# Kernel optimization log

Hardware: AMD Instinct MI355X
Metric: run time of the kernel (lower is better)

## Reference

```python
import jax, jax.numpy as jnp
import numpy as np
from jax import lax

BN_EPS = 1e-3
SLOPE = 0.1
CLUSTER_TEMP = 30.0
K = 16
FEAT = 4096  # 8*8*64


def conv_bn_lrelu(x, w, b, g, beta, m, v):
    # Conv2d stride 2, padding 1 (NCHW / OIHW), then eval-mode BatchNorm, then LeakyReLU.
    y = lax.conv_general_dilated(x, w, window_strides=(2, 2), padding=((1, 1), (1, 1)),
                                 dimension_numbers=("NCHW", "OIHW", "NCHW"))
    y = y + b[None, :, None, None]
    scale = g / jnp.sqrt(v + BN_EPS)
    y = y * scale[None, :, None, None] + (beta - m * scale)[None, :, None, None]
    return jnp.where(y > 0, y, SLOPE * y)


def soft_kmeans(data, mu, num_iter, ct):
    # Row L2-normalize (equivalent to diag(1/||x||) @ data)
    data = data / jnp.linalg.norm(data, axis=1, keepdims=True)
    for _ in range(num_iter):
        dist = data @ mu.T                      # [N, K]
        r = jax.nn.softmax(ct * dist, axis=1)   # [N, K]
        mu = (r.T @ data) / r.sum(axis=0)[:, None]  # [K, F]
    dist = data @ mu.T
    r = jax.nn.softmax(ct * dist, axis=1)
    return mu, r, dist


def setup_inputs() -> dict:
    key = jax.random.key(0)
    ks = jax.random.split(key, 12)
    d = {}
    d["x"] = jax.random.normal(ks[0], (256, 3, 64, 64), dtype=jnp.float32)
    # conv1: 3 -> 128
    d["conv1_w"] = jax.random.normal(ks[1], (128, 3, 3, 3), dtype=jnp.float32) * 0.05
    d["conv1_b"] = jnp.zeros((128,), jnp.float32)
    d["bn1_g"] = jnp.ones((128,), jnp.float32)
    d["bn1_b"] = jnp.zeros((128,), jnp.float32)
    d["bn1_m"] = jax.random.normal(ks[2], (128,), dtype=jnp.float32) * 0.1
    d["bn1_v"] = jax.random.uniform(ks[3], (128,), minval=0.5, maxval=1.5, dtype=jnp.float32)
    # conv2: 128 -> 256
    d["conv2_w"] = jax.random.normal(ks[4], (256, 128, 3, 3), dtype=jnp.float32) * 0.02
    d["conv2_b"] = jnp.zeros((256,), jnp.float32)
    d["bn2_g"] = jnp.ones((256,), jnp.float32)
    d["bn2_b"] = jnp.zeros((256,), jnp.float32)
    d["bn2_m"] = jax.random.normal(ks[5], (256,), dtype=jnp.float32) * 0.1
    d["bn2_v"] = jax.random.uniform(ks[6], (256,), minval=0.5, maxval=1.5, dtype=jnp.float32)
    # conv3: 256 -> 64
    d["conv3_w"] = jax.random.normal(ks[7], (64, 256, 3, 3), dtype=jnp.float32) * 0.02
    d["conv3_b"] = jnp.zeros((64,), jnp.float32)
    d["bn3_g"] = jnp.ones((64,), jnp.float32)
    d["bn3_b"] = jnp.zeros((64,), jnp.float32)
    d["bn3_m"] = jax.random.normal(ks[8], (64,), dtype=jnp.float32) * 0.1
    d["bn3_v"] = jax.random.uniform(ks[9], (64,), minval=0.5, maxval=1.5, dtype=jnp.float32)
    # initial cluster centers, torch.rand(K, F)
    d["mu0"] = jax.random.uniform(ks[10], (K, FEAT), dtype=jnp.float32)
    d["num_iter"] = 10
    return d


def reference(x, conv1_w, conv1_b, bn1_g, bn1_b, bn1_m, bn1_v,
              conv2_w, conv2_b, bn2_g, bn2_b, bn2_m, bn2_v,
              conv3_w, conv3_b, bn3_g, bn3_b, bn3_m, bn3_v,
              mu0, num_iter):
    h = conv_bn_lrelu(x, conv1_w, conv1_b, bn1_g, bn1_b, bn1_m, bn1_v)   # [B,128,32,32]
    h = conv_bn_lrelu(h, conv2_w, conv2_b, bn2_g, bn2_b, bn2_m, bn2_v)   # [B,256,16,16]
    h = conv_bn_lrelu(h, conv3_w, conv3_b, bn3_g, bn3_b, bn3_m, bn3_v)   # [B,64,8,8]
    embeds = h.reshape(-1, FEAT)                                          # [B, 4096]
    mu_init, _, _ = soft_kmeans(embeds, mu0, num_iter, CLUSTER_TEMP)
    _, r, _ = soft_kmeans(embeds, lax.stop_gradient(mu_init), 1, CLUSTER_TEMP)
    return r
```

## Files before the change

kernel.cpp:

```cpp
#include <hip/hip_runtime.h>
#include <stdint.h>
#include <stddef.h>

typedef unsigned short u16;
typedef __attribute__((ext_vector_type(8))) short short8;
typedef __attribute__((ext_vector_type(4))) float f32x4;
typedef __attribute__((ext_vector_type(4))) int int4v;

__device__ __forceinline__ float bf2f(u16 u) {
    unsigned x = ((unsigned)u) << 16;
    return __uint_as_float(x);
}
__device__ __forceinline__ u16 f2bf(float f) {
    unsigned x = __float_as_uint(f);
    unsigned r = (x + 0x7fffu + ((x >> 16) & 1u)) >> 16;
    return (u16)r;
}
__device__ __forceinline__ float ldin(const void* p, size_t i, int isbf) {
    return isbf ? bf2f(((const u16*)p)[i]) : ((const float*)p)[i];
}
__device__ __forceinline__ int detect_bf(const void* v1) {
    const u16* ub = (const u16*)v1;
    int ok = 1;
#pragma unroll
    for (int i = 0; i < 16; i++) {
        float f = bf2f(ub[i]);
        if (!(f >= 0.4f && f <= 1.6f)) ok = 0;
    }
    return ok;
}
__device__ __forceinline__ int sw(int r, int c8) {
    return r * 32 + (((c8) ^ (r & 3)) << 3);
}

struct PrepArgs {
    const void *w1, *w2, *w3;
    u16 *W1p, *W2p, *W3p;
    const void *b1, *g1, *be1, *m1, *v1;
    const void *b2, *g2, *be2, *m2, *v2;
    const void *b3, *g3, *be3, *m3, *v3;
    float *es1, *esh1, *es2, *esh2, *es3, *esh3;
    u16 *zb;
};
__device__ __forceinline__ void packw_body(const void* src, u16* dst, int CI, int Kp,
                                           int total, int blk, int t, int isbf) {
    int p = blk * 256 + t;
    if (p >= total) return;
    int co = p / Kp, k = p - co * Kp;
    int tap = k / CI, ci = k - tap * CI;
    u16 v = 0;
    if (tap < 9) {
        size_t si = (size_t)(co * CI + ci) * 9 + tap;
        v = isbf ? ((const u16*)src)[si] : f2bf(((const float*)src)[si]);
    }
    dst[p] = v;
}
__global__ __launch_bounds__(256) void kprep_all(PrepArgs A) {
    int b = blockIdx.x, t = threadIdx.x;
    int isbf = detect_bf(A.v1);
    if (b < 1152) {
        packw_body(A.w2, A.W2p, 128, 1152, 256 * 1152, b, t, isbf);
    } else if (b < 1728) {
        packw_body(A.w3, A.W3p, 256, 2304, 64 * 2304, b - 1152, t, isbf);
    } else if (b < 1744) {
        packw_body(A.w1, A.W1p, 3, 32, 128 * 32, b - 1728, t, isbf);
    } else {
        if (b == 1745) A.zb[t] = 0;
        int u = (b - 1744) * 256 + t;
        const void *bb, *g, *be, *m, *v;
        float *es, *esh;
        int c;
        if (u < 128)      { c = u;       bb=A.b1; g=A.g1; be=A.be1; m=A.m1; v=A.v1; es=A.es1; esh=A.esh1; }
        else if (u < 384) { c = u - 128; bb=A.b2; g=A.g2; be=A.be2; m=A.m2; v=A.v2; es=A.es2; esh=A.esh2; }
        else if (u < 448) { c = u - 384; bb=A.b3; g=A.g3; be=A.be3; m=A.m3; v=A.v3; es=A.es3; esh=A.esh3; }
        else return;
        float sc = ldin(g, c, isbf) / sqrtf(ldin(v, c, isbf) + 1e-3f);
        float sh = (ldin(bb, c, isbf) - ldin(m, c, isbf)) * sc + ldin(be, c, isbf);
        es[c] = sc;
        esh[c] = sh;
    }
}

__global__ void kfallback(u16* __restrict__ out) {
    int i = blockIdx.x * 256 + threadIdx.x;
    if (i < 4096) out[i] = f2bf(0.0625f);
}

__global__ __launch_bounds__(256) void imc1_gemm(
    const void* __restrict__ x, const u16* __restrict__ W,
    const float* __restrict__ es, const float* __restrict__ esh,
    u16* __restrict__ OutB, const void* __restrict__ v1ref) {
    __shared__ u16 xs[3 * 64 * 64];
    alignas(16) __shared__ u16 As[2][128 * 32];
    alignas(16) __shared__ u16 Bs[128 * 32];

    const int img = blockIdx.x, t = threadIdx.x;
    const int isbf = detect_bf(v1ref);
    const int lane = t & 63, w = t >> 6;
    const int wm = w & 1, wn = w >> 1;
    const int rA = t >> 2, c8 = t & 3, koff = c8 * 8;
    const int qc = lane >> 4, fr = lane & 15;

    if (isbf) {
        const u16* xp = (const u16*)x + (size_t)img * 12288;
#pragma unroll
        for (int i = t * 8; i < 12288; i += 2048)
            *(int4v*)&xs[i] = *(const int4v*)&xp[i];
    } else {
        const float* xp = (const float*)x + (size_t)img * 12288;
#pragma unroll
        for (int i = t * 4; i < 12288; i += 1024) {
            float4 v = *(const float4*)&xp[i];
            xs[i] = f2bf(v.x); xs[i + 1] = f2bf(v.y);
            xs[i + 2] = f2bf(v.z); xs[i + 3] = f2bf(v.w);
        }
    }
#pragma unroll
    for (int j = 0; j < 2; j++) {
        int4v vb = *(const int4v*)(W + (size_t)(j * 64 + rA) * 32 + koff);
        *(int4v*)&Bs[sw(j * 64 + rA, c8)] = vb;
    }
    __syncthreads();
    short8 bf[4];
#pragma unroll
    for (int j = 0; j < 4; j++) bf[j] = *(const short8*)&Bs[sw(wn * 64 + j * 16 + fr, qc)];
    float scv[4], shv[4];
#pragma unroll
    for (int j = 0; j < 4; j++) {
        int c = wn * 64 + j * 16 + fr;
        scv[j] = es[c];
        shv[j] = esh[c];
    }

    for (int sub = 0; sub < 8; ++sub) {
        const int buf = sub & 1;
#pragma unroll
        for (int j = 0; j < 2; j++) {
            int r = j * 64 + rA;
            int p = sub * 128 + r;
            int ox = p & 31, oy = p >> 5;
            alignas(16) u16 row[8];
#pragma unroll
            for (int e = 0; e < 8; e++) {
                int k = koff + e;
                u16 val = 0;
                if (k < 27) {
                    int tap = k / 3, ci = k - 3 * tap;
                    int ky = tap / 3, kx = tap - 3 * ky;
                    int iy = 2 * oy - 1 + ky, ix = 2 * ox - 1 + kx;
                    if ((unsigned)iy < 64u && (unsigned)ix < 64u)
                        val = xs[ci * 4096 + iy * 64 + ix];
                }
                row[e] = val;
            }
            *(int4v*)&As[buf][sw(r, c8)] = *(const int4v*)row;
        }
        __syncthreads();
        short8 af[4];
#pragma unroll
        for (int i = 0; i < 4; i++)
            af[i] = *(const short8*)&As[buf][sw(wm * 64 + i * 16 + fr, qc)];
        f32x4 acc[4][4];
#pragma unroll
        for (int i = 0; i < 4; i++)
#pragma unroll
            for (int j = 0; j < 4; j++) {
#pragma unroll
                for (int q = 0; q < 4; q++) acc[i][j][q] = 0.f;
                acc[i][j] = __builtin_amdgcn_mfma_f32_16x16x32_bf16(af[i], bf[j], acc[i][j], 0, 0, 0);
            }
#pragma unroll
        for (int i = 0; i < 4; i++) {
#pragma unroll
            for (int rg = 0; rg < 4; rg++) {
                int p = sub * 128 + wm * 64 + i * 16 + qc * 4 + rg;
                int ox = p & 31, oy = p >> 5;
                u16* orow = OutB + ((size_t)(img * 32 + oy) * 32 + ox) * 128 + wn * 64 + fr;
#pragma unroll
                for (int j = 0; j < 4; j++) {
                    float v = acc[i][j][rg] * scv[j] + shv[j];
                    v = (v > 0.f) ? v : 0.1f * v;
                    orow[j * 16] = f2bf(v);
                }
            }
        }
    }
}

__global__ __launch_bounds__(512, 2) void gemm_conv2(
    const u16* __restrict__ h1, const u16* __restrict__ W,
    const float* __restrict__ es, const float* __restrict__ esh,
    u16* __restrict__ OutB, const u16* __restrict__ zb) {
    alignas(16) __shared__ u16 smem[4 * 16384];
    u16* const Ab0 = smem;
    u16* const Ab1 = smem + 16384;
    u16* const Bb0 = smem + 32768;
    u16* const Bb1 = smem + 49152;

    const int t = threadIdx.x;
    const int w = t >> 6, l = t & 63;
    const int img = blockIdx.x;
    const int wm = w >> 2, wn = w & 3;
    const int fr = l & 15, qc = l >> 4;

    int aiy0[4], aix0[4], ac8e[4];
    int brow[4];
#pragma unroll
    for (int i = 0; i < 4; ++i) {
        int gi = w * 256 + i * 64 + l;
        int r = gi >> 3, c8d = gi & 7;
        int c8s = c8d ^ (r & 7);
        int oy = r >> 4, ox = r & 15;
        aiy0[i] = 2 * oy - 1;
        aix0[i] = 2 * ox - 1;
        ac8e[i] = c8s * 8;
        brow[i] = r * 1152 + c8s * 8;
    }
    auto mkA = [&](int i, int ky, int kx) -> const u16* {
        int iy = aiy0[i] + ky, ix = aix0[i] + kx;
        if ((unsigned)iy < 32u && (unsigned)ix < 32u)
            return h1 + (size_t)(((img * 32 + iy) * 32 + ix) * 128 + ac8e[i]);
        return zb;
    };
    auto stage = [&](const u16* src, u16* ldsbase, int i) {
        __builtin_amdgcn_global_load_lds(
            (const __attribute__((address_space(1))) void*)src,
            (__attribute__((address_space(3))) void*)(ldsbase + (w * 4 + i) * 512),
            16, 0, 0);
    };

    f32x4 acc[8][4];
#pragma unroll
    for (int mi = 0; mi < 8; ++mi)
#pragma unroll
        for (int nj = 0; nj < 4; ++nj)
#pragma unroll
            for (int q = 0; q < 4; ++q) acc[mi][nj][q] = 0.0f;

    auto do_tile = [&](const u16* A, const u16* B) {
#pragma unroll
        for (int kk = 0; kk < 2; ++kk) {
            const int c8 = kk * 4 + qc;
            short8 a[8], b[4];
#pragma unroll
            for (int q = 0; q < 8; ++q) {
                int row = wm * 128 + q * 16 + fr;
                a[q] = *(const short8*)(A + row * 64 + ((c8 ^ (row & 7)) << 3));
            }
#pragma unroll
            for (int j = 0; j < 4; ++j) {
                int row = wn * 64 + j * 16 + fr;
                b[j] = *(const short8*)(B + row * 64 + ((c8 ^ (row & 7)) << 3));
            }
            __builtin_amdgcn_s_setprio(1);
#pragma unroll
            for (int q = 0; q < 8; ++q)
#pragma unroll
                for (int j = 0; j < 4; ++j)
                    acc[q][j] = __builtin_amdgcn_mfma_f32_16x16x32_bf16(
                        a[q], b[j], acc[q][j], 0, 0, 0);
            __builtin_amdgcn_s_setprio(0);
        }
    };

    const u16* pcur[4];
#pragma unroll
    for (int i = 0; i < 4; ++i) pcur[i] = mkA(i, 0, 0);
#pragma unroll
    for (int i = 0; i < 4; ++i) {
        stage(pcur[i], Ab0, i);
        stage(W + brow[i], Bb0, i);
    }

    for (int tap = 0; tap < 9; ++tap) {
        __syncthreads();
#pragma unroll
        for (int i = 0; i < 4; ++i) {
            stage(pcur[i] + 64, Ab1, i);
            stage(W + brow[i] + (2 * tap + 1) * 64, Bb1, i);
        }
        do_tile(Ab0, Bb0);
        __syncthreads();
        if (tap < 8) {
            const int tap2 = tap + 1;
            const int ky2 = (tap2 >= 6) ? 2 : (tap2 >= 3) ? 1 : 0;
            const int kx2 = tap2 - 3 * ky2;
#pragma unroll
            for (int i = 0; i < 4; ++i) pcur[i] = mkA(i, ky2, kx2);
#pragma unroll
            for (int i = 0; i < 4; ++i) {
                stage(pcur[i], Ab0, i);
                stage(W + brow[i] + (2 * tap + 2) * 64, Bb0, i);
            }
        }
        do_tile(Ab1, Bb1);
    }

    float scv[4], shv[4];
#pragma unroll
    for (int nj = 0; nj < 4; ++nj) {
        int c = wn * 64 + nj * 16 + fr;
        scv[nj] = es[c];
        shv[nj] = esh[c];
    }
#pragma unroll
    for (int mi = 0; mi < 8; ++mi) {
#pragma unroll
        for (int rg = 0; rg < 4; ++rg) {
            int r = wm * 128 + mi * 16 + qc * 4 + rg;
            u16* orow = OutB + ((size_t)img * 256 + r) * 256 + wn * 64 + fr;
#pragma unroll
            for (int nj = 0; nj < 4; ++nj) {
                float v = acc[mi][nj][rg] * scv[nj] + shv[nj];
                v = (v > 0.f) ? v : 0.1f * v;
                orow[nj * 16] = f2bf(v);
            }
        }
    }
}

__global__ __launch_bounds__(256) void gemm_conv3f(
    const u16* __restrict__ Asrc, const u16* __restrict__ W,
    const float* __restrict__ es3, const float* __restrict__ esh3,
    float* __restrict__ dat, u16* __restrict__ datbf,
    const u16* __restrict__ zb) {
    alignas(16) __shared__ u16 smem[4 * 4096];
    __shared__ float red[4];
    u16* const AbP[2] = {smem, smem + 4096};
    u16* const BbP[2] = {smem + 8192, smem + 12288};

    const int t = threadIdx.x;
    const int w = t >> 6, l = t & 63;
    const int lid = blockIdx.x;
    const int xcd = lid & 7, slot = lid >> 3;
    const int img = xcd * 32 + slot;
    const int wm = w & 1, wn = w >> 1;
    const int fr = l & 15, qc = l >> 4;

    int aiy0[2], aix0[2], ac8e[2];
    int brow[2];
#pragma unroll
    for (int i = 0; i < 2; ++i) {
        int g = w * 128 + i * 64 + l;
        int r = g >> 3, c8d = g & 7;
        int c8s = c8d ^ (r & 7);
        int oy = r >> 3, ox = r & 7;
        aiy0[i] = 2 * oy - 1;
        aix0[i] = 2 * ox - 1;
        ac8e[i] = c8s * 8;
        brow[i] = r * 2304 + c8s * 8;
    }
    auto mkA = [&](int i, int ky, int kx) -> const u16* {
        int iy = aiy0[i] + ky, ix = aix0[i] + kx;
        if ((unsigned)iy < 16u && (unsigned)ix < 16u)
            return Asrc + (size_t)(((img * 16 + iy) * 16 + ix) * 256 + ac8e[i]);
        return zb;
    };
    auto stage = [&](const u16* src, u16* ldsbase, int i) {
        __builtin_amdgcn_global_load_lds(
            (const __attribute__((address_space(1))) void*)src,
            (__attribute__((address_space(3))) void*)(ldsbase + (w * 2 + i) * 512),
            16, 0, 0);
    };

    f32x4 acc[2][2];
#pragma unroll
    for (int i = 0; i < 2; i++)
#pragma unroll
        for (int j = 0; j < 2; j++)
#pragma unroll
            for (int q = 0; q < 4; q++) acc[i][j][q] = 0.0f;

    auto do_tile = [&](const u16* A, const u16* B) {
#pragma unroll
        for (int kk = 0; kk < 2; ++kk) {
            const int c8 = kk * 4 + qc;
            short8 a[2], b[2];
#pragma unroll
            for (int i = 0; i < 2; ++i) {
                int row = wm * 32 + i * 16 + fr;
                a[i] = *(const short8*)(A + row * 64 + ((c8 ^ (row & 7)) << 3));
            }
#pragma unroll
            for (int j = 0; j < 2; ++j) {
                int row = wn * 32 + j * 16 + fr;
                b[j] = *(const short8*)(B + row * 64 + ((c8 ^ (row & 7)) << 3));
            }
            __builtin_amdgcn_s_setprio(1);
#pragma unroll
            for (int i = 0; i < 2; ++i)
#pragma unroll
                for (int j = 0; j < 2; ++j)
                    acc[i][j] = __builtin_amdgcn_mfma_f32_16x16x32_bf16(
                        a[i], b[j], acc[i][j], 0, 0, 0);
            __builtin_amdgcn_s_setprio(0);
        }
    };

    const u16* pcur[2];
#pragma unroll
    for (int i = 0; i < 2; ++i) pcur[i] = mkA(i, 0, 0);
#pragma unroll
    for (int i = 0; i < 2; ++i) {
        stage(pcur[i], AbP[0], i);
        stage(W + brow[i], BbP[0], i);
    }

    int flat = 0;
    for (int tap = 0; tap < 9; ++tap) {
        for (int q4 = 0; q4 < 4; ++q4, ++flat) {
            const int cb = flat & 1;
            __syncthreads();
            int ntap = tap, nq = q4 + 1;
            if (nq == 4) { nq = 0; ntap = tap + 1; }
            if (ntap < 9) {
                if (nq == 0) {
                    const int ky = (ntap >= 6) ? 2 : (ntap >= 3) ? 1 : 0;
                    const int kx = ntap - 3 * ky;
#pragma unroll
                    for (int i = 0; i < 2; ++i) pcur[i] = mkA(i, ky, kx);
                }
#pragma unroll
                for (int i = 0; i < 2; ++i) {
                    stage(pcur[i] + nq * 64, AbP[cb ^ 1], i);
                    stage(W + brow[i] + ntap * 256 + nq * 64, BbP[cb ^ 1], i);
                }
            }
            do_tile(AbP[cb], BbP[cb]);
        }
    }

    float vals[2][2][4];
    float ssq = 0.f;
#pragma unroll
    for (int j = 0; j < 2; j++) {
        int c = wn * 32 + j * 16 + fr;
        float sc = es3[c], sh = esh3[c];
#pragma unroll
        for (int i = 0; i < 2; i++) {
#pragma unroll
            for (int rg = 0; rg < 4; rg++) {
                float v = acc[i][j][rg] * sc + sh;
                v = (v > 0.f) ? v : 0.1f * v;
                vals[i][j][rg] = v;
                ssq += v * v;
            }
        }
    }
#pragma unroll
    for (int off = 32; off > 0; off >>= 1) ssq += __shfl_xor(ssq, off);
    if (l == 0) red[w] = ssq;
    __syncthreads();
    float inv = 1.0f / sqrtf(red[0] + red[1] + red[2] + red[3]);
#pragma unroll
    for (int j = 0; j < 2; j++) {
        int c = wn * 32 + j * 16 + fr;
#pragma unroll
        for (int i = 0; i < 2; i++) {
#pragma unroll
            for (int rg = 0; rg < 4; rg++) {
                int row = wm * 32 + i * 16 + qc * 4 + rg;
                size_t idx = (size_t)img * 4096 + c * 64 + row;
                float v = vals[i][j][rg] * inv;
                dat[idx] = v;
                datbf[idx] = f2bf(v);
            }
        }
    }
}

__global__ __launch_bounds__(256) void kgr(const u16* __restrict__ dbf,
                                           const float* __restrict__ dat,
                                           const void* __restrict__ mu0,
                                           float* __restrict__ Gp,
                                           float* __restrict__ rb0,
                                           const void* __restrict__ v1ref) {
    const int b = blockIdx.x, t = threadIdx.x;
    __shared__ float part[16][4];
    __shared__ float ds[16];

    if (b < 128) {
        const int tile = b & 15, s = b >> 4;
        const int m0 = (tile & 3) * 64, n0 = (tile >> 2) * 64;
        const int lane = t & 63, w = t >> 6;
        const int wm = w & 1, wn = w >> 1;
        const int fr = lane & 15, qc = lane >> 4;

        f32x4 acc[2][2];
#pragma unroll
        for (int i = 0; i < 2; i++)
#pragma unroll
            for (int j = 0; j < 2; j++)
#pragma unroll
                for (int q = 0; q < 4; q++) acc[i][j][q] = 0.0f;

        const u16* a0p = dbf + (size_t)(m0 + wm * 32 + fr) * 4096 + s * 512 + qc * 8;
        const u16* a1p = a0p + 16 * 4096;
        const u16* b0p = dbf + (size_t)(n0 + wn * 32 + fr) * 4096 + s * 512 + qc * 8;
        const u16* b1p = b0p + 16 * 4096;

        short8 Pa0[4], Pa1[4], Pb0[4], Pb1[4];
        short8 Qa0[4], Qa1[4], Qb0[4], Qb1[4];
        auto ldc = [&](short8* A0, short8* A1, short8* B0, short8* B1, int c) {
#pragma unroll
            for (int u = 0; u < 4; ++u) {
                const int o = c * 128 + u * 32;
                A0[u] = *(const short8*)(a0p + o);
                A1[u] = *(const short8*)(a1p + o);
                B0[u] = *(const short8*)(b0p + o);
                B1[u] = *(const short8*)(b1p + o);
            }
        };
        auto mmc = [&](short8* A0, short8* A1, short8* B0, short8* B1) {
#pragma unroll
            for (int u = 0; u < 4; ++u) {
                acc[0][0] = __builtin_amdgcn_mfma_f32_16x16x32_bf16(A0[u], B0[u], acc[0][0], 0, 0, 0);
                acc[0][1] = __builtin_amdgcn_mfma_f32_16x16x32_bf16(A0[u], B1[u], acc[0][1], 0, 0, 0);
                acc[1][0] = __builtin_amdgcn_mfma_f32_16x16x32_bf16(A1[u], B0[u], acc[1][0], 0, 0, 0);
                acc[1][1] = __builtin_amdgcn_mfma_f32_16x16x32_bf16(A1[u], B1[u], acc[1][1], 0, 0, 0);
            }
        };
        ldc(Pa0, Pa1, Pb0, Pb1, 0);
#pragma unroll
        for (int c = 0; c < 2; ++c) {
            ldc(Qa0, Qa1, Qb0, Qb1, 2 * c + 1);
            mmc(Pa0, Pa1, Pb0, Pb1);
            if (c < 1) ldc(Pa0, Pa1, Pb0, Pb1, 2 * c + 2);
            mmc(Qa0, Qa1, Qb0, Qb1);
        }

        float* gp = Gp + (size_t)s * 65536;
#pragma unroll
        for (int j = 0; j < 2; j++) {
            int cc = n0 + wn * 32 + j * 16 + fr;
#pragma unroll
            for (int i = 0; i < 2; i++)
#pragma unroll
                for (int rg = 0; rg < 4; rg++) {
                    int row = m0 + wm * 32 + i * 16 + qc * 4 + rg;
                    gp[row * 256 + cc] = acc[i][j][rg];
                }
        }
    } else {
        const int n = b - 128;
        const int isbf = detect_bf(v1ref);
        const int lane = t & 63, wv = t >> 6;
        float d[16];
#pragma unroll
        for (int j = 0; j < 16; j++) d[j] = dat[(size_t)n * 4096 + j * 256 + t];
#pragma unroll
        for (int k = 0; k < 16; k++) {
            float a = 0.f;
            if (isbf) {
                const u16* mp = (const u16*)mu0 + (size_t)k * 4096;
#pragma unroll
                for (int j = 0; j < 16; j++) a = fmaf(d[j], bf2f(mp[j * 256 + t]), a);
            } else {
                const float* mp = (const float*)mu0 + (size_t)k * 4096;
#pragma unroll
                for (int j = 0; j < 16; j++) a = fmaf(d[j], mp[j * 256 + t], a);
            }
#pragma unroll
            for (int off = 32; off > 0; off >>= 1) a += __shfl_xor(a, off);
            if (lane == 0) part[k][wv] = a;
        }
        __syncthreads();
        if (t < 16) {
            float dk = part[t][0] + part[t][1] + part[t][2] + part[t][3];
            ds[t] = dk;
            __syncthreads();
            float mx = -1e30f;
#pragma unroll
            for (int j = 0; j < 16; j++) mx = fmaxf(mx, ds[j]);
            float sum = 0.f;
#pragma unroll
            for (int j = 0; j < 16; j++) sum += __expf(30.f * (ds[j] - mx));
            rb0[n * 16 + t] = __expf(30.f * (dk - mx)) / sum;
        }
    }
}

__global__ __launch_bounds__(256) void kcomb(const float* __restrict__ Gp,
                                             u16* __restrict__ Ghi,
                                             u16* __restrict__ Glo) {
    const int i = (blockIdx.x * 256 + threadIdx.x) * 4;
    f32x4 s[8];
#pragma unroll
    for (int p = 0; p < 8; p++) s[p] = *(const f32x4*)(Gp + (size_t)p * 65536 + i);
    unsigned long long ph = 0, pl = 0;
#pragma unroll
    for (int q = 0; q < 4; q++) {
        float v = s[0][q];
#pragma unroll
        for (int p = 1; p < 8; p++) v += s[p][q];
        u16 hi = f2bf(v);
        u16 lo = f2bf(v - bf2f(hi));
        ph |= ((unsigned long long)hi) << (16 * q);
        pl |= ((unsigned long long)lo) << (16 * q);
    }
    *(unsigned long long*)(Ghi + i) = ph;
    *(unsigned long long*)(Glo + i) = pl;
}

__global__ __launch_bounds__(512) void kmiter(const u16* __restrict__ Ghi,
                                              const u16* __restrict__ Glo,
                                              const float* __restrict__ rb0,
                                              void* __restrict__ dout,
                                              const void* __restrict__ v1ref) {
    const int t = threadIdx.x;
    const int isbf = detect_bf(v1ref);
    const int lane = t & 63, w = t >> 6;
    const int i0 = w * 32;
    const int col = lane & 15;
    const int q = lane >> 4;

    __shared__ u16 rThi[2][16 * 264];
    __shared__ u16 rTlo[2][16 * 264];
    __shared__ float part[2][8][17];

    short8 gh[2][8], gl[2][8];
#pragma unroll
    for (int sg = 0; sg < 2; sg++) {
        const u16* Ah = Ghi + (size_t)(i0 + sg * 16 + col) * 256 + q * 8;
        const u16* Al = Glo + (size_t)(i0 + sg * 16 + col) * 256 + q * 8;
#pragma unroll
        for (int s = 0; s < 8; s++) {
            gh[sg][s] = *(const short8*)(Ah + s * 32);
            gl[sg][s] = *(const short8*)(Al + s * 32);
        }
    }

    {
        float rv[2][4];
#pragma unroll
        for (int sg = 0; sg < 2; sg++)
#pragma unroll
            for (int rg = 0; rg < 4; rg++) {
                int row = i0 + sg * 16 + q * 4 + rg;
                float v = rb0[row * 16 + col];
                rv[sg][rg] = v;
                u16 hi = f2bf(v);
                rThi[0][col * 264 + row] = hi;
                rTlo[0][col * 264 + row] = f2bf(v - bf2f(hi));
            }
        float s0 = (rv[0][0] + rv[0][1] + rv[0][2] + rv[0][3]) +
                   (rv[1][0] + rv[1][1] + rv[1][2] + rv[1][3]);
        s0 += __shfl_xor(s0, 16);
        s0 += __shfl_xor(s0, 32);
        if (lane < 16) part[0][w][lane] = s0;
    }
    __syncthreads();
    float rsc = 0.f;
#pragma unroll
    for (int ww = 0; ww < 8; ww++) rsc += part[0][ww][col];

    int cur = 0;
    for (int iter = 0; iter < 11; iter++) {
        f32x4 a0[2] = {{0.f, 0.f, 0.f, 0.f}, {0.f, 0.f, 0.f, 0.f}};
        f32x4 a1[2] = {{0.f, 0.f, 0.f, 0.f}, {0.f, 0.f, 0.f, 0.f}};
#pragma unroll
        for (int s = 0; s < 4; s++) {
            short8 bh = *(const short8*)&rThi[cur][col * 264 + s * 32 + q * 8];
            short8 bl = *(const short8*)&rTlo[cur][col * 264 + s * 32 + q * 8];
#pragma unroll
            for (int sg = 0; sg < 2; sg++) {
                a0[sg] = __builtin_amdgcn_mfma_f32_16x16x32_bf16(gh[sg][s], bh, a0[sg], 0, 0, 0);
                a0[sg] = __builtin_amdgcn_mfma_f32_16x16x32_bf16(gl[sg][s], bh, a0[sg], 0, 0, 0);
                a0[sg] = __builtin_amdgcn_mfma_f32_16x16x32_bf16(gh[sg][s], bl, a0[sg], 0, 0, 0);
            }
            short8 bh2 = *(const short8*)&rThi[cur][col * 264 + (s + 4) * 32 + q * 8];
            short8 bl2 = *(const short8*)&rTlo[cur][col * 264 + (s + 4) * 32 + q * 8];
#pragma unroll
            for (int sg = 0; sg < 2; sg++) {
                a1[sg] = __builtin_amdgcn_mfma_f32_16x16x32_bf16(gh[sg][s + 4], bh2, a1[sg], 0, 0, 0);
                a1[sg] = __builtin_amdgcn_mfma_f32_16x16x32_bf16(gl[sg][s + 4], bh2, a1[sg], 0, 0, 0);
                a1[sg] = __builtin_amdgcn_mfma_f32_16x16x32_bf16(gh[sg][s + 4], bl2, a1[sg], 0, 0, 0);
            }
        }
        float nv[2][4];
#pragma unroll
        for (int sg = 0; sg < 2; sg++)
#pragma unroll
            for (int rg = 0; rg < 4; rg++) {
                float dk = (a0[sg][rg] + a1[sg][rg]) / rsc;
                float mx = dk;
#pragma unroll
                for (int o = 1; o < 16; o <<= 1) mx = fmaxf(mx, __shfl_xor(mx, o));
                float e = __expf(30.f * (dk - mx));
                float ssum = e;
#pragma unroll
                for (int o = 1; o < 16; o <<= 1) ssum += __shfl_xor(ssum, o);
                nv[sg][rg] = e / ssum;
            }
        if (iter < 10) {
            const int nxt = cur ^ 1;
#pragma unroll
            for (int sg = 0; sg < 2; sg++)
#pragma unroll
                for (int rg = 0; rg < 4; rg++) {
                    int row = i0 + sg * 16 + q * 4 + rg;
                    u16 hi = f2bf(nv[sg][rg]);
                    rThi[nxt][col * 264 + row] = hi;
                    rTlo[nxt][col * 264 + row] = f2bf(nv[sg][rg] - bf2f(hi));
                }
            float s0 = (nv[0][0] + nv[0][1] + nv[0][2] + nv[0][3]) +
                       (nv[1][0] + nv[1][1] + nv[1][2] + nv[1][3]);
            s0 += __shfl_xor(s0, 16);
            s0 += __shfl_xor(s0, 32);
            if (lane < 16) part[nxt][w][lane] = s0;
            __syncthreads();
            rsc = 0.f;
#pragma unroll
            for (int ww = 0; ww < 8; ww++) rsc += part[nxt][ww][col];
            cur = nxt;
        } else {
#pragma unroll
            for (int sg = 0; sg < 2; sg++)
#pragma unroll
                for (int rg = 0; rg < 4; rg++) {
                    int row = i0 + sg * 16 + q * 4 + rg;
                    if (isbf) ((u16*)dout)[row * 16 + col] = f2bf(nv[sg][rg]);
                    else ((float*)dout)[row * 16 + col] = nv[sg][rg];
                }
        }
    }
}

extern "C" void kernel_launch(void* const* d_in, const int* in_sizes, int n_in,
                              void* d_out, int out_size, void* d_ws, size_t ws_size,
                              hipStream_t stream) {
    const void* x   = d_in[0];
    const void* w1  = d_in[1];
    const void* b1  = d_in[2];
    const void* g1  = d_in[3];
    const void* be1 = d_in[4];
    const void* m1  = d_in[5];
    const void* v1  = d_in[6];
    const void* w2  = d_in[7];
    const void* b2  = d_in[8];
    const void* g2  = d_in[9];
    const void* be2 = d_in[10];
    const void* m2  = d_in[11];
    const void* v2  = d_in[12];
    const void* w3  = d_in[13];
    const void* b3  = d_in[14];
    const void* g3  = d_in[15];
    const void* be3 = d_in[16];
    const void* m3  = d_in[17];
    const void* v3  = d_in[18];
    const void* mu0 = d_in[19];

    char* p = (char*)d_ws;
    size_t used = 0;
    auto alloc = [&](size_t bytes) -> char* {
        char* q = p;
        size_t rb = (bytes + 255) & ~(size_t)255;
        p += rb;
        used += rb;
        return q;
    };
    float* rb0 = (float*)alloc(4096 * 4);
    u16* Ghi = (u16*)alloc((size_t)65536 * 2);
    u16* Glo = (u16*)alloc((size_t)65536 * 2);
    float* Gp = (float*)alloc((size_t)8 * 65536 * 4);
    u16* W1p = (u16*)alloc((size_t)128 * 32 * 2);
    u16* W2p = (u16*)alloc((size_t)256 * 1152 * 2);
    u16* W3p = (u16*)alloc((size_t)64 * 2304 * 2);
    float* es1 = (float*)alloc(128 * 4);
    float* esh1 = (float*)alloc(128 * 4);
    float* es2 = (float*)alloc(256 * 4);
    float* esh2 = (float*)alloc(256 * 4);
    float* es3 = (float*)alloc(64 * 4);
    float* esh3 = (float*)alloc(64 * 4);
    u16* zb = (u16*)alloc(512);
    const size_t R1 = (size_t)256 * 32 * 32 * 128 * 2;
    const size_t R2 = (size_t)256 * 16 * 16 * 256 * 2;
    char* reg1 = alloc(R1);
    char* reg2 = alloc(R2);
    u16* h1 = (u16*)reg1;
    u16* h2 = (u16*)reg2;
    float* dat = (float*)reg1;
    u16* datbf = (u16*)(reg1 + 4194304);

    if (used > ws_size) {
        kfallback<<<16, 256, 0, stream>>>((u16*)d_out);
        return;
    }

    PrepArgs pa = {w1, w2, w3, W1p, W2p, W3p,
                   b1, g1, be1, m1, v1, b2, g2, be2, m2, v2, b3, g3, be3, m3, v3,
                   es1, esh1, es2, esh2, es3, esh3, zb};
    kprep_all<<<1746, 256, 0, stream>>>(pa);
    imc1_gemm<<<dim3(256), 256, 0, stream>>>(x, W1p, es1, esh1, h1, v1);
    gemm_conv2<<<dim3(256), 512, 0, stream>>>(h1, W2p, es2, esh2, h2, zb);
    gemm_conv3f<<<dim3(256), 256, 0, stream>>>(h2, W3p, es3, esh3, dat, datbf, zb);
    kgr<<<dim3(384), 256, 0, stream>>>(datbf, dat, mu0, Gp, rb0, v1);
    kcomb<<<dim3(64), 256, 0, stream>>>(Gp, Ghi, Glo);
    kmiter<<<1, 512, 0, stream>>>(Ghi, Glo, rb0, d_out, v1);
}
```

Measured before the change: 246.0 us.

## Fuse conv1 and conv2 into a single per-image kernel

```diff
diff --git a/kernel.cpp b/kernel.cpp
--- a/kernel.cpp
+++ b/kernel.cpp
@@ -86,120 +86,130 @@
     if (i < 4096) out[i] = f2bf(0.0625f);
 }
 
-__global__ __launch_bounds__(256) void imc1_gemm(
-    const void* __restrict__ x, const u16* __restrict__ W,
-    const float* __restrict__ es, const float* __restrict__ esh,
-    u16* __restrict__ OutB, const void* __restrict__ v1ref) {
-    __shared__ u16 xs[3 * 64 * 64];
-    alignas(16) __shared__ u16 As[2][128 * 32];
-    alignas(16) __shared__ u16 Bs[128 * 32];
-
-    const int img = blockIdx.x, t = threadIdx.x;
-    const int isbf = detect_bf(v1ref);
-    const int lane = t & 63, w = t >> 6;
-    const int wm = w & 1, wn = w >> 1;
-    const int rA = t >> 2, c8 = t & 3, koff = c8 * 8;
-    const int qc = lane >> 4, fr = lane & 15;
-
-    if (isbf) {
-        const u16* xp = (const u16*)x + (size_t)img * 12288;
-#pragma unroll
-        for (int i = t * 8; i < 12288; i += 2048)
-            *(int4v*)&xs[i] = *(const int4v*)&xp[i];
-    } else {
-        const float* xp = (const float*)x + (size_t)img * 12288;
-#pragma unroll
-        for (int i = t * 4; i < 12288; i += 1024) {
-            float4 v = *(const float4*)&xp[i];
-            xs[i] = f2bf(v.x); xs[i + 1] = f2bf(v.y);
-            xs[i + 2] = f2bf(v.z); xs[i + 3] = f2bf(v.w);
-        }
-    }
-#pragma unroll
-    for (int j = 0; j < 2; j++) {
-        int4v vb = *(const int4v*)(W + (size_t)(j * 64 + rA) * 32 + koff);
-        *(int4v*)&Bs[sw(j * 64 + rA, c8)] = vb;
+__global__ __launch_bounds__(512, 2) void conv12(
+    const void* __restrict__ x, const u16* __restrict__ W1,
+    const float* __restrict__ es1, const float* __restrict__ esh1,
+    const u16* __restrict__ W2, const float* __restrict__ es2,
+    const float* __restrict__ esh2, u16* __restrict__ h1,
+    u16* __restrict__ OutB, const u16* __restrict__ zb,
+    const void* __restrict__ v1ref) {
+    alignas(16) __shared__ u16 smem[65536];
+
+    const int t = threadIdx.x;
+    const int img = blockIdx.x;
+
+    {
+        u16* const xs = smem;
+        u16* const As2 = smem + 12288;
+        u16* const Bs = smem + 12288 + 16384;
+        const int isbf = detect_bf(v1ref);
+
+        if (isbf) {
+            const u16* xp = (const u16*)x + (size_t)img * 12288;
+#pragma unroll
+            for (int i = t * 8; i < 12288; i += 4096)
+                *(int4v*)&xs[i] = *(const int4v*)&xp[i];
+        } else {
+            const float* xp = (const float*)x + (size_t)img * 12288;
+#pragma unroll
+            for (int i = t * 4; i < 12288; i += 2048) {
+                float4 v = *(const float4*)&xp[i];
+                xs[i] = f2bf(v.x); xs[i + 1] = f2bf(v.y);
+                xs[i + 2] = f2bf(v.z); xs[i + 3] = f2bf(v.w);
+            }
+        }
+        if (t < 256) {
+            const int rA = t >> 2, c8 = t & 3, koff = c8 * 8;
+#pragma unroll
+            for (int j = 0; j < 2; j++) {
+                int4v vb = *(const int4v*)(W1 + (size_t)(j * 64 + rA) * 32 + koff);
+                *(int4v*)&Bs[sw(j * 64 + rA, c8)] = vb;
+            }
+        }
+        __syncthreads();
+
+        const int hh = t >> 8;
+        const int g = t & 255;
+        const int lane = g & 63, w4 = g >> 6;
+        const int wm = w4 & 1, wn = w4 >> 1;
+        const int rA = g >> 2, c8 = g & 3, koff = c8 * 8;
+        const int qc = lane >> 4, fr = lane & 15;
+        u16* const As_h = As2 + hh * 8192;
+
+        short8 bf[4];
+#pragma unroll
+        for (int j = 0; j < 4; j++) bf[j] = *(const short8*)&Bs[sw(wn * 64 + j * 16 + fr, qc)];
+        float scv[4], shv[4];
+#pragma unroll
+        for (int j = 0; j < 4; j++) {
+            int c = wn * 64 + j * 16 + fr;
+            scv[j] = es1[c];
+            shv[j] = esh1[c];
+        }
+
+        for (int it = 0; it < 4; ++it) {
+            const int sub = it * 2 + hh;
+            u16* const As = As_h + (it & 1) * 4096;
+#pragma unroll
+            for (int j = 0; j < 2; j++) {
+                int r = j * 64 + rA;
+                int p = sub * 128 + r;
+                int ox = p & 31, oy = p >> 5;
+                alignas(16) u16 row[8];
+#pragma unroll
+                for (int e = 0; e < 8; e++) {
+                    int k = koff + e;
+                    u16 val = 0;
+                    if (k < 27) {
+                        int tap = k / 3, ci = k - 3 * tap;
+                        int ky = tap / 3, kx = tap - 3 * ky;
+                        int iy = 2 * oy - 1 + ky, ix = 2 * ox - 1 + kx;
+                        if ((unsigned)iy < 64u && (unsigned)ix < 64u)
+                            val = xs[ci * 4096 + iy * 64 + ix];
+                    }
+                    row[e] = val;
+                }
+                *(int4v*)&As[sw(r, c8)] = *(const int4v*)row;
+            }
+            __syncthreads();
+            short8 af[4];
+#pragma unroll
+            for (int i = 0; i < 4; i++)
+                af[i] = *(const short8*)&As[sw(wm * 64 + i * 16 + fr, qc)];
+            f32x4 acc[4][4];
+#pragma unroll
+            for (int i = 0; i < 4; i++)
+#pragma unroll
+                for (int j = 0; j < 4; j++) {
+#pragma unroll
+                    for (int q = 0; q < 4; q++) acc[i][j][q] = 0.f;
+                    acc[i][j] = __builtin_amdgcn_mfma_f32_16x16x32_bf16(af[i], bf[j], acc[i][j], 0, 0, 0);
+                }
+#pragma unroll
+            for (int i = 0; i < 4; i++) {
+#pragma unroll
+                for (int rg = 0; rg < 4; rg++) {
+                    int p = sub * 128 + wm * 64 + i * 16 + qc * 4 + rg;
+                    int ox = p & 31, oy = p >> 5;
+                    u16* orow = h1 + ((size_t)(img * 32 + oy) * 32 + ox) * 128 + wn * 64 + fr;
+#pragma unroll
+                    for (int j = 0; j < 4; j++) {
+                        float v = acc[i][j][rg] * scv[j] + shv[j];
+                        v = (v > 0.f) ? v : 0.1f * v;
+                        orow[j * 16] = f2bf(v);
+                    }
+                }
+            }
+        }
     }
     __syncthreads();
-    short8 bf[4];
-#pragma unroll
-    for (int j = 0; j < 4; j++) bf[j] = *(const short8*)&Bs[sw(wn * 64 + j * 16 + fr, qc)];
-    float scv[4], shv[4];
-#pragma unroll
-    for (int j = 0; j < 4; j++) {
-        int c = wn * 64 + j * 16 + fr;
-        scv[j] = es[c];
-        shv[j] = esh[c];
-    }
-
-    for (int sub = 0; sub < 8; ++sub) {
-        const int buf = sub & 1;
-#pragma unroll
-        for (int j = 0; j < 2; j++) {
-            int r = j * 64 + rA;
-            int p = sub * 128 + r;
-            int ox = p & 31, oy = p >> 5;
-            alignas(16) u16 row[8];
-#pragma unroll
-            for (int e = 0; e < 8; e++) {
-                int k = koff + e;
-                u16 val = 0;
-                if (k < 27) {
-                    int tap = k / 3, ci = k - 3 * tap;
-                    int ky = tap / 3, kx = tap - 3 * ky;
-                    int iy = 2 * oy - 1 + ky, ix = 2 * ox - 1 + kx;
-                    if ((unsigned)iy < 64u && (unsigned)ix < 64u)
-                        val = xs[ci * 4096 + iy * 64 + ix];
-                }
-                row[e] = val;
-            }
-            *(int4v*)&As[buf][sw(r, c8)] = *(const int4v*)row;
-        }
-        __syncthreads();
-        short8 af[4];
-#pragma unroll
-        for (int i = 0; i < 4; i++)
-            af[i] = *(const short8*)&As[buf][sw(wm * 64 + i * 16 + fr, qc)];
-        f32x4 acc[4][4];
-#pragma unroll
-        for (int i = 0; i < 4; i++)
-#pragma unroll
-            for (int j = 0; j < 4; j++) {
-#pragma unroll
-                for (int q = 0; q < 4; q++) acc[i][j][q] = 0.f;
-                acc[i][j] = __builtin_amdgcn_mfma_f32_16x16x32_bf16(af[i], bf[j], acc[i][j], 0, 0, 0);
-            }
-#pragma unroll
-        for (int i = 0; i < 4; i++) {
-#pragma unroll
-            for (int rg = 0; rg < 4; rg++) {
-                int p = sub * 128 + wm * 64 + i * 16 + qc * 4 + rg;
-                int ox = p & 31, oy = p >> 5;
-                u16* orow = OutB + ((size_t)(img * 32 + oy) * 32 + ox) * 128 + wn * 64 + fr;
-#pragma unroll
-                for (int j = 0; j < 4; j++) {
-                    float v = acc[i][j][rg] * scv[j] + shv[j];
-                    v = (v > 0.f) ? v : 0.1f * v;
-                    orow[j * 16] = f2bf(v);
-                }
-            }
-        }
-    }
-}
-
-__global__ __launch_bounds__(512, 2) void gemm_conv2(
-    const u16* __restrict__ h1, const u16* __restrict__ W,
-    const float* __restrict__ es, const float* __restrict__ esh,
-    u16* __restrict__ OutB, const u16* __restrict__ zb) {
-    alignas(16) __shared__ u16 smem[4 * 16384];
+
     u16* const Ab0 = smem;
     u16* const Ab1 = smem + 16384;
     u16* const Bb0 = smem + 32768;
     u16* const Bb1 = smem + 49152;
 
-    const int t = threadIdx.x;
     const int w = t >> 6, l = t & 63;
-    const int img = blockIdx.x;
     const int wm = w >> 2, wn = w & 3;
     const int fr = l & 15, qc = l >> 4;
 
@@ -269,7 +279,7 @@
 #pragma unroll
     for (int i = 0; i < 4; ++i) {
         stage(pcur[i], Ab0, i);
-        stage(W + brow[i], Bb0, i);
+        stage(W2 + brow[i], Bb0, i);
     }
 
     for (int tap = 0; tap < 9; ++tap) {
@@ -277,7 +287,7 @@
 #pragma unroll
         for (int i = 0; i < 4; ++i) {
             stage(pcur[i] + 64, Ab1, i);
-            stage(W + brow[i] + (2 * tap + 1) * 64, Bb1, i);
+            stage(W2 + brow[i] + (2 * tap + 1) * 64, Bb1, i);
         }
         do_tile(Ab0, Bb0);
         __syncthreads();
@@ -290,7 +300,7 @@
 #pragma unroll
             for (int i = 0; i < 4; ++i) {
                 stage(pcur[i], Ab0, i);
-                stage(W + brow[i] + (2 * tap + 2) * 64, Bb0, i);
+                stage(W2 + brow[i] + (2 * tap + 2) * 64, Bb0, i);
             }
         }
         do_tile(Ab1, Bb1);
@@ -300,8 +310,8 @@
 #pragma unroll
     for (int nj = 0; nj < 4; ++nj) {
         int c = wn * 64 + nj * 16 + fr;
-        scv[nj] = es[c];
-        shv[nj] = esh[c];
+        scv[nj] = es2[c];
+        shv[nj] = esh2[c];
     }
 #pragma unroll
     for (int mi = 0; mi < 8; ++mi) {
@@ -791,8 +801,8 @@
                    b1, g1, be1, m1, v1, b2, g2, be2, m2, v2, b3, g3, be3, m3, v3,
                    es1, esh1, es2, esh2, es3, esh3, zb};
     kprep_all<<<1746, 256, 0, stream>>>(pa);
-    imc1_gemm<<<dim3(256), 256, 0, stream>>>(x, W1p, es1, esh1, h1, v1);
-    gemm_conv2<<<dim3(256), 512, 0, stream>>>(h1, W2p, es2, esh2, h2, zb);
+    conv12<<<dim3(256), 512, 0, stream>>>(x, W1p, es1, esh1, W2p, es2, esh2,
+                                          h1, h2, zb, v1);
     gemm_conv3f<<<dim3(256), 256, 0, stream>>>(h2, W3p, es3, esh3, dat, datbf, zb);
     kgr<<<dim3(384), 256, 0, stream>>>(datbf, dat, mu0, Gp, rb0, v1);
     kcomb<<<dim3(64), 256, 0, stream>>>(Gp, Ghi, Glo);
```

New measurement: 249.2 us. Within noise of the previous version (+1.3%).
